# Optimization experiments

Measured on AMD Instinct MI355X. Metric: run time of the kernel, lower is better.

Reference implementation:

```python
import jax, jax.numpy as jnp
import numpy as np

ALPHA = 0.2
EMB_DIM = 128
IMG = 48


def setup_inputs() -> dict:
    key = jax.random.key(0)
    k1, k2, k3, k4 = jax.random.split(key, 4)
    B = 8192
    batch_anchor = jax.random.normal(k1, (B, 1, IMG, IMG), dtype=jnp.float32)
    batch_pos = jax.random.normal(k2, (B, 1, IMG, IMG), dtype=jnp.float32)
    batch_neg = jax.random.normal(k3, (B, 1, IMG, IMG), dtype=jnp.float32)
    W = jax.random.normal(k4, (IMG * IMG, EMB_DIM), dtype=jnp.float32) * (1.0 / np.sqrt(IMG * IMG))
    b = jnp.zeros((EMB_DIM,), dtype=jnp.float32)
    return {"batch_anchor": batch_anchor, "batch_pos": batch_pos, "batch_neg": batch_neg, "W": W, "b": b}


def _encode(x, W, b):
    # x: [B, 1, 48, 48] -> flatten -> linear -> [B, emb]
    B = x.shape[0]
    return x.reshape(B, -1) @ W + b


def reference(batch_anchor, batch_pos, batch_neg, W, b):
    emb_a = _encode(batch_anchor, W, b)
    emb_p = _encode(batch_pos, W, b)
    emb_n = _encode(batch_neg, W, b)
    d_ap = jnp.sum((emb_a - emb_p) ** 2, axis=-1)  # squared distance, [B]
    d_an = jnp.sum((emb_a - emb_n) ** 2, axis=-1)
    loss = jax.nn.relu(d_ap - d_an + ALPHA)
    return jnp.mean(loss)
```

## Files before the change

### kernel.cpp

```cpp
#include <hip/hip_runtime.h>


#define KDIM  2304
#define EMBD  128
#define BATCH 8192
#define NT    8
#define NW    8
#define CPW   9
#define ALPHA 0.2f

typedef __attribute__((ext_vector_type(8))) short short8;
typedef __attribute__((ext_vector_type(4))) float f32x4;
typedef __attribute__((ext_vector_type(4))) unsigned int u32x4;

#define AS1 __attribute__((address_space(1)))
#define AS3 __attribute__((address_space(3)))

__device__ __forceinline__ unsigned short f2bf(float f) {
    unsigned u = __builtin_bit_cast(unsigned, f);
    u += 0x7FFFu + ((u >> 16) & 1u);
    return (unsigned short)(u >> 16);
}

__global__ void pack_w_kernel(const float* __restrict__ W,
                              unsigned short* __restrict__ Wp) {
    int tid = blockIdx.x * blockDim.x + threadIdx.x;
    int n = tid & 127;
    int k = tid >> 7;
    int c = k >> 5;
    int q = (k >> 3) & 3;
    int j = k & 7;
    int t = n >> 4;
    int l = q * 16 + (n & 15);
    Wp[(size_t)(((c * 8 + t) * 64) + l) * 8 + j] = f2bf(W[tid]);
}

__device__ __forceinline__ unsigned cvtpk(float lo, float hi) {
    unsigned r;
    asm("v_cvt_pk_bf16_f32 %0, %1, %2" : "=v"(r) : "v"(lo), "v"(hi));
    return r;
}

__device__ __forceinline__ void gll16(const float* g, char* l) {
    __builtin_amdgcn_global_load_lds((AS1 void*)(void*)g, (AS3 void*)l, 16, 0, 0);
}

__device__ __forceinline__ void lds_read6(const char* p, f32x4& a0, f32x4& a1,
                                          f32x4& p0, f32x4& p1,
                                          f32x4& n0, f32x4& n1) {
    const AS3 char* lp = (const AS3 char*)p;
    asm volatile(
        "ds_read_b128 %0, %6 offset:0\n\t"
        "ds_read_b128 %1, %6 offset:1024\n\t"
        "ds_read_b128 %2, %6 offset:2048\n\t"
        "ds_read_b128 %3, %6 offset:3072\n\t"
        "ds_read_b128 %4, %6 offset:4096\n\t"
        "ds_read_b128 %5, %6 offset:5120\n\t"
        "s_waitcnt lgkmcnt(0)"
        : "=&v"(a0), "=&v"(a1), "=&v"(p0), "=&v"(p1), "=&v"(n0), "=&v"(n1)
        : "v"(lp)
        : "memory");
}

__global__ __launch_bounds__(512, 2) void triplet_kernel(
    const float* __restrict__ A, const float* __restrict__ P,
    const float* __restrict__ Ng, const unsigned short* __restrict__ Wp,
    float* __restrict__ out)
{
    __shared__ __align__(16) char smem[NW * 12288];

    const int lane = threadIdx.x & 63;
    const int wave = threadIdx.x >> 6;
    const int c0   = wave * CPW;

    const size_t goff = (size_t)(blockIdx.x * 16 + (lane & 15)) * KDIM
                      + (size_t)(lane >> 4) * 8 + (size_t)c0 * 32;
    const float* gA = A  + goff;
    const float* gP = P  + goff;
    const float* gN = Ng + goff;

    char* wb = smem + wave * 12288;

    const short8* wp = (const short8*)Wp + lane + (size_t)c0 * NT * 64;

    f32x4 aU[NT], aV[NT];
#pragma unroll
    for (int t = 0; t < NT; ++t) {
        aU[t] = (f32x4){0.f, 0.f, 0.f, 0.f};
        aV[t] = (f32x4){0.f, 0.f, 0.f, 0.f};
    }

#define STAGE(cc, bufoff)                                   \
    do {                                                    \
        const float* _a = gA + (cc) * 32;                   \
        const float* _p = gP + (cc) * 32;                   \
        const float* _n = gN + (cc) * 32;                   \
        char* _b = wb + (bufoff);                           \
        gll16(_a,     _b);                                  \
        gll16(_a + 4, _b + 1024);                           \
        gll16(_p,     _b + 2048);                           \
        gll16(_p + 4, _b + 3072);                           \
        gll16(_n,     _b + 4096);                           \
        gll16(_n + 4, _b + 5120);                           \
    } while (0)

    STAGE(0, 0);

    const char* rp0 = wb + lane * 16;
    const char* rp1 = wb + 6144 + lane * 16;

#pragma unroll
    for (int c = 0; c < CPW; ++c) {
        short8 wf[NT];
#pragma unroll
        for (int t = 0; t < NT; ++t) wf[t] = wp[c * 512 + t * 64];

        if (c + 1 < CPW) {
            STAGE(c + 1, ((c + 1) & 1) * 6144);
            asm volatile("s_waitcnt vmcnt(6)" ::: "memory");
        } else {
            asm volatile("s_waitcnt vmcnt(0)" ::: "memory");
        }

        f32x4 xa0, xa1, xp0, xp1, xn0, xn1;
        lds_read6((c & 1) ? rp1 : rp0, xa0, xa1, xp0, xp1, xn0, xn1);

        f32x4 ul = xa0 - xp0, uh = xa1 - xp1;
        f32x4 vl = xa0 - xn0, vh = xa1 - xn1;
        u32x4 uw, vw;
        uw[0] = cvtpk(ul[0], ul[1]); uw[1] = cvtpk(ul[2], ul[3]);
        uw[2] = cvtpk(uh[0], uh[1]); uw[3] = cvtpk(uh[2], uh[3]);
        vw[0] = cvtpk(vl[0], vl[1]); vw[1] = cvtpk(vl[2], vl[3]);
        vw[2] = cvtpk(vh[0], vh[1]); vw[3] = cvtpk(vh[2], vh[3]);
        short8 uf = __builtin_bit_cast(short8, uw);
        short8 vf = __builtin_bit_cast(short8, vw);

#pragma unroll
        for (int t = 0; t < NT; ++t) {
            aU[t] = __builtin_amdgcn_mfma_f32_16x16x32_bf16(uf, wf[t], aU[t], 0, 0, 0);
            aV[t] = __builtin_amdgcn_mfma_f32_16x16x32_bf16(vf, wf[t], aV[t], 0, 0, 0);
        }
    }

    __syncthreads();

    float (*lds)[2][NT][64][4] = (float(*)[2][NT][64][4])(void*)smem;

#define STORE_FRAGS(r)                                              \
    do {                                                            \
        _Pragma("unroll")                                           \
        for (int t = 0; t < NT; ++t) {                              \
            *(f32x4*)&lds[r][0][t][lane][0] = aU[t];                \
            *(f32x4*)&lds[r][1][t][lane][0] = aV[t];                \
        }                                                           \
    } while (0)
#define ADD_FRAGS(r)                                                \
    do {                                                            \
        _Pragma("unroll")                                           \
        for (int t = 0; t < NT; ++t) {                              \
            aU[t] += *(const f32x4*)&lds[r][0][t][lane][0];         \
            aV[t] += *(const f32x4*)&lds[r][1][t][lane][0];         \
        }                                                           \
    } while (0)

    if (wave >= 4) STORE_FRAGS(wave - 4);
    __syncthreads();
    if (wave < 4) ADD_FRAGS(wave);
    __syncthreads();
    if (wave == 2 || wave == 3) STORE_FRAGS(wave - 2);
    __syncthreads();
    if (wave < 2) ADD_FRAGS(wave);
    __syncthreads();
    if (wave == 1) STORE_FRAGS(0);
    __syncthreads();

    if (wave == 0) {
        ADD_FRAGS(0);
        float du[4] = {0.f, 0.f, 0.f, 0.f};
        float dv[4] = {0.f, 0.f, 0.f, 0.f};
#pragma unroll
        for (int t = 0; t < NT; ++t) {
#pragma unroll
            for (int r = 0; r < 4; ++r) {
                du[r] += aU[t][r] * aU[t][r];
                dv[r] += aV[t][r] * aV[t][r];
            }
        }
#pragma unroll
        for (int msk = 1; msk < 16; msk <<= 1) {
#pragma unroll
            for (int r = 0; r < 4; ++r) {
                du[r] += __shfl_xor(du[r], msk, 64);
                dv[r] += __shfl_xor(dv[r], msk, 64);
            }
        }
        float s = 0.f;
#pragma unroll
        for (int r = 0; r < 4; ++r) {
            float l = du[r] - dv[r] + ALPHA;
            s += l > 0.f ? l : 0.f;
        }
        s += __shfl_xor(s, 16, 64);
        s += __shfl_xor(s, 32, 64);
        if (lane == 0) atomicAdd(out, s * (1.0f / BATCH));
    }
}

extern "C" void kernel_launch(void* const* d_in, const int* in_sizes, int n_in,
                              void* d_out, int out_size, void* d_ws, size_t ws_size,
                              hipStream_t stream) {
    const float* A  = (const float*)d_in[0];
    const float* P  = (const float*)d_in[1];
    const float* Ng = (const float*)d_in[2];
    const float* W  = (const float*)d_in[3];
    unsigned short* Wp = (unsigned short*)d_ws;

    hipMemsetAsync(d_out, 0, sizeof(float), stream);

    pack_w_kernel<<<(KDIM * EMBD) / 256, 256, 0, stream>>>(W, Wp);
    triplet_kernel<<<BATCH / 16, 512, 0, stream>>>(A, P, Ng, Wp, (float*)d_out);
}
```

Measured before the change: 236.4 us.

## Process two row tiles per wave to reuse W fragments across rows

Each block now handles 32 batch rows with 4 waves instead of 16 rows with 8 waves, and each wave splits K into 18 chunks and computes two 16-row M-tiles. Every W fragment loaded from global memory is reused for two MFMA tiles, which halves W traffic per row, and the cross-wave LDS reduction loses one stage. In exchange the accumulator count doubles, so register pressure rises, launch bounds drop to one block per SM, and the grid shrinks to 256 blocks, which cuts occupancy and latency hiding for the streaming input loads.

New measurement: 234.5 us. About the same (-0.8%).

```diff
diff --git a/kernel.cpp b/kernel.cpp
--- a/kernel.cpp
+++ b/kernel.cpp
@@ -5,8 +5,9 @@
 #define EMBD  128
 #define BATCH 8192
 #define NT    8
-#define NW    8
-#define CPW   9
+#define NW    4
+#define MT    2
+#define CPW   18
 #define ALPHA 0.2f
 
 typedef __attribute__((ext_vector_type(8))) short short8;
@@ -62,52 +63,56 @@
         : "memory");
 }
 
-__global__ __launch_bounds__(512, 2) void triplet_kernel(
+__global__ __launch_bounds__(256, 1) void triplet_kernel(
     const float* __restrict__ A, const float* __restrict__ P,
     const float* __restrict__ Ng, const unsigned short* __restrict__ Wp,
     float* __restrict__ out)
 {
-    __shared__ __align__(16) char smem[NW * 12288];
+    __shared__ __align__(16) char smem[NW * 24576];
 
     const int lane = threadIdx.x & 63;
     const int wave = threadIdx.x >> 6;
     const int c0   = wave * CPW;
 
-    const size_t goff = (size_t)(blockIdx.x * 16 + (lane & 15)) * KDIM
-                      + (size_t)(lane >> 4) * 8 + (size_t)c0 * 32;
-    const float* gA = A  + goff;
-    const float* gP = P  + goff;
-    const float* gN = Ng + goff;
-
-    char* wb = smem + wave * 12288;
+    const size_t goff0 = (size_t)(blockIdx.x * 32 + (lane & 15)) * KDIM
+                       + (size_t)(lane >> 4) * 8 + (size_t)c0 * 32;
+    const size_t goff1 = goff0 + (size_t)16 * KDIM;
+    const float* gA0 = A  + goff0;  const float* gA1 = A  + goff1;
+    const float* gP0 = P  + goff0;  const float* gP1 = P  + goff1;
+    const float* gN0 = Ng + goff0;  const float* gN1 = Ng + goff1;
+
+    char* wb = smem + wave * 24576;
 
     const short8* wp = (const short8*)Wp + lane + (size_t)c0 * NT * 64;
 
-    f32x4 aU[NT], aV[NT];
-#pragma unroll
-    for (int t = 0; t < NT; ++t) {
-        aU[t] = (f32x4){0.f, 0.f, 0.f, 0.f};
-        aV[t] = (f32x4){0.f, 0.f, 0.f, 0.f};
-    }
+    f32x4 aU[MT][NT], aV[MT][NT];
+#pragma unroll
+    for (int mt = 0; mt < MT; ++mt)
+#pragma unroll
+        for (int t = 0; t < NT; ++t) {
+            aU[mt][t] = (f32x4){0.f, 0.f, 0.f, 0.f};
+            aV[mt][t] = (f32x4){0.f, 0.f, 0.f, 0.f};
+        }
 
 #define STAGE(cc, bufoff)                                   \
     do {                                                    \
-        const float* _a = gA + (cc) * 32;                   \
-        const float* _p = gP + (cc) * 32;                   \
-        const float* _n = gN + (cc) * 32;                   \
+        const int _o = (cc) * 32;                           \
         char* _b = wb + (bufoff);                           \
-        gll16(_a,     _b);                                  \
-        gll16(_a + 4, _b + 1024);                           \
-        gll16(_p,     _b + 2048);                           \
-        gll16(_p + 4, _b + 3072);                           \
-        gll16(_n,     _b + 4096);                           \
-        gll16(_n + 4, _b + 5120);                           \
+        gll16(gA0 + _o,     _b);                            \
+        gll16(gA0 + _o + 4, _b + 1024);                     \
+        gll16(gP0 + _o,     _b + 2048);                     \
+        gll16(gP0 + _o + 4, _b + 3072);                     \
+        gll16(gN0 + _o,     _b + 4096);                     \
+        gll16(gN0 + _o + 4, _b + 5120);                     \
+        gll16(gA1 + _o,     _b + 6144);                     \
+        gll16(gA1 + _o + 4, _b + 7168);                     \
+        gll16(gP1 + _o,     _b + 8192);                     \
+        gll16(gP1 + _o + 4, _b + 9216);                     \
+        gll16(gN1 + _o,     _b + 10240);                    \
+        gll16(gN1 + _o + 4, _b + 11264);                    \
     } while (0)
 
     STAGE(0, 0);
-
-    const char* rp0 = wb + lane * 16;
-    const char* rp1 = wb + 6144 + lane * 16;
 
 #pragma unroll
     for (int c = 0; c < CPW; ++c) {
@@ -116,58 +121,62 @@
         for (int t = 0; t < NT; ++t) wf[t] = wp[c * 512 + t * 64];
 
         if (c + 1 < CPW) {
-            STAGE(c + 1, ((c + 1) & 1) * 6144);
-            asm volatile("s_waitcnt vmcnt(6)" ::: "memory");
+            STAGE(c + 1, ((c + 1) & 1) * 12288);
+            asm volatile("s_waitcnt vmcnt(12)" ::: "memory");
         } else {
             asm volatile("s_waitcnt vmcnt(0)" ::: "memory");
         }
 
-        f32x4 xa0, xa1, xp0, xp1, xn0, xn1;
-        lds_read6((c & 1) ? rp1 : rp0, xa0, xa1, xp0, xp1, xn0, xn1);
-
-        f32x4 ul = xa0 - xp0, uh = xa1 - xp1;
-        f32x4 vl = xa0 - xn0, vh = xa1 - xn1;
-        u32x4 uw, vw;
-        uw[0] = cvtpk(ul[0], ul[1]); uw[1] = cvtpk(ul[2], ul[3]);
-        uw[2] = cvtpk(uh[0], uh[1]); uw[3] = cvtpk(uh[2], uh[3]);
-        vw[0] = cvtpk(vl[0], vl[1]); vw[1] = cvtpk(vl[2], vl[3]);
-        vw[2] = cvtpk(vh[0], vh[1]); vw[3] = cvtpk(vh[2], vh[3]);
-        short8 uf = __builtin_bit_cast(short8, uw);
-        short8 vf = __builtin_bit_cast(short8, vw);
-
-#pragma unroll
-        for (int t = 0; t < NT; ++t) {
-            aU[t] = __builtin_amdgcn_mfma_f32_16x16x32_bf16(uf, wf[t], aU[t], 0, 0, 0);
-            aV[t] = __builtin_amdgcn_mfma_f32_16x16x32_bf16(vf, wf[t], aV[t], 0, 0, 0);
+#pragma unroll
+        for (int mt = 0; mt < MT; ++mt) {
+            const char* rp = wb + (c & 1) * 12288 + mt * 6144 + lane * 16;
+            f32x4 xa0, xa1, xp0, xp1, xn0, xn1;
+            lds_read6(rp, xa0, xa1, xp0, xp1, xn0, xn1);
+
+            f32x4 ul = xa0 - xp0, uh = xa1 - xp1;
+            f32x4 vl = xa0 - xn0, vh = xa1 - xn1;
+            u32x4 uw, vw;
+            uw[0] = cvtpk(ul[0], ul[1]); uw[1] = cvtpk(ul[2], ul[3]);
+            uw[2] = cvtpk(uh[0], uh[1]); uw[3] = cvtpk(uh[2], uh[3]);
+            vw[0] = cvtpk(vl[0], vl[1]); vw[1] = cvtpk(vl[2], vl[3]);
+            vw[2] = cvtpk(vh[0], vh[1]); vw[3] = cvtpk(vh[2], vh[3]);
+            short8 uf = __builtin_bit_cast(short8, uw);
+            short8 vf = __builtin_bit_cast(short8, vw);
+
+#pragma unroll
+            for (int t = 0; t < NT; ++t) {
+                aU[mt][t] = __builtin_amdgcn_mfma_f32_16x16x32_bf16(uf, wf[t], aU[mt][t], 0, 0, 0);
+                aV[mt][t] = __builtin_amdgcn_mfma_f32_16x16x32_bf16(vf, wf[t], aV[mt][t], 0, 0, 0);
+            }
         }
     }
 
     __syncthreads();
 
-    float (*lds)[2][NT][64][4] = (float(*)[2][NT][64][4])(void*)smem;
+    float (*lds)[MT][2][NT][64][4] = (float(*)[MT][2][NT][64][4])(void*)smem;
 
 #define STORE_FRAGS(r)                                              \
     do {                                                            \
         _Pragma("unroll")                                           \
-        for (int t = 0; t < NT; ++t) {                              \
-            *(f32x4*)&lds[r][0][t][lane][0] = aU[t];                \
-            *(f32x4*)&lds[r][1][t][lane][0] = aV[t];                \
-        }                                                           \
+        for (int mt = 0; mt < MT; ++mt)                             \
+        { _Pragma("unroll")                                         \
+          for (int t = 0; t < NT; ++t) {                            \
+            *(f32x4*)&lds[r][mt][0][t][lane][0] = aU[mt][t];        \
+            *(f32x4*)&lds[r][mt][1][t][lane][0] = aV[mt][t];        \
+          } }                                                       \
     } while (0)
 #define ADD_FRAGS(r)                                                \
     do {                                                            \
         _Pragma("unroll")                                           \
-        for (int t = 0; t < NT; ++t) {                              \
-            aU[t] += *(const f32x4*)&lds[r][0][t][lane][0];         \
-            aV[t] += *(const f32x4*)&lds[r][1][t][lane][0];         \
-        }                                                           \
+        for (int mt = 0; mt < MT; ++mt)                             \
+        { _Pragma("unroll")                                         \
+          for (int t = 0; t < NT; ++t) {                            \
+            aU[mt][t] += *(const f32x4*)&lds[r][mt][0][t][lane][0]; \
+            aV[mt][t] += *(const f32x4*)&lds[r][mt][1][t][lane][0]; \
+          } }                                                       \
     } while (0)
 
-    if (wave >= 4) STORE_FRAGS(wave - 4);
-    __syncthreads();
-    if (wave < 4) ADD_FRAGS(wave);
-    __syncthreads();
-    if (wave == 2 || wave == 3) STORE_FRAGS(wave - 2);
+    if (wave >= 2) STORE_FRAGS(wave - 2);
     __syncthreads();
     if (wave < 2) ADD_FRAGS(wave);
     __syncthreads();
@@ -176,30 +185,37 @@
 
     if (wave == 0) {
         ADD_FRAGS(0);
-        float du[4] = {0.f, 0.f, 0.f, 0.f};
-        float dv[4] = {0.f, 0.f, 0.f, 0.f};
-#pragma unroll
-        for (int t = 0; t < NT; ++t) {
+        float du[MT][4], dv[MT][4];
+#pragma unroll
+        for (int mt = 0; mt < MT; ++mt)
+#pragma unroll
+            for (int r = 0; r < 4; ++r) { du[mt][r] = 0.f; dv[mt][r] = 0.f; }
+#pragma unroll
+        for (int mt = 0; mt < MT; ++mt)
+#pragma unroll
+            for (int t = 0; t < NT; ++t)
+#pragma unroll
+                for (int r = 0; r < 4; ++r) {
+                    du[mt][r] += aU[mt][t][r] * aU[mt][t][r];
+                    dv[mt][r] += aV[mt][t][r] * aV[mt][t][r];
+                }
+#pragma unroll
+        for (int msk = 1; msk < 16; msk <<= 1)
+#pragma unroll
+            for (int mt = 0; mt < MT; ++mt)
+#pragma unroll
+                for (int r = 0; r < 4; ++r) {
+                    du[mt][r] += __shfl_xor(du[mt][r], msk, 64);
+                    dv[mt][r] += __shfl_xor(dv[mt][r], msk, 64);
+                }
+        float s = 0.f;
+#pragma unroll
+        for (int mt = 0; mt < MT; ++mt)
 #pragma unroll
             for (int r = 0; r < 4; ++r) {
-                du[r] += aU[t][r] * aU[t][r];
-                dv[r] += aV[t][r] * aV[t][r];
+                float l = du[mt][r] - dv[mt][r] + ALPHA;
+                s += l > 0.f ? l : 0.f;
             }
-        }
-#pragma unroll
-        for (int msk = 1; msk < 16; msk <<= 1) {
-#pragma unroll
-            for (int r = 0; r < 4; ++r) {
-                du[r] += __shfl_xor(du[r], msk, 64);
-                dv[r] += __shfl_xor(dv[r], msk, 64);
-            }
-        }
-        float s = 0.f;
-#pragma unroll
-        for (int r = 0; r < 4; ++r) {
-            float l = du[r] - dv[r] + ALPHA;
-            s += l > 0.f ? l : 0.f;
-        }
         s += __shfl_xor(s, 16, 64);
         s += __shfl_xor(s, 32, 64);
         if (lane == 0) atomicAdd(out, s * (1.0f / BATCH));
@@ -218,5 +234,5 @@
     hipMemsetAsync(d_out, 0, sizeof(float), stream);
 
     pack_w_kernel<<<(KDIM * EMBD) / 256, 256, 0, stream>>>(W, Wp);
-    triplet_kernel<<<BATCH / 16, 512, 0, stream>>>(A, P, Ng, Wp, (float*)d_out);
-}
+    triplet_kernel<<<BATCH / 32, 256, 0, stream>>>(A, P, Ng, Wp, (float*)d_out);
+}
```

## Switch to 32x32x16 MFMA tiles with 32 rows per block and double-buffered W fragments

Applied to the files above, without the earlier changes.

Each block now handles 32 batch rows using 32x32x16 bf16 MFMAs over 4 output tiles, with 18 K-chunks per wave instead of 9. Each W fragment loaded from global memory is reused across twice as many rows, and the next chunk's W fragments are prefetched into a second register set alongside the LDS staging of the inputs. The cross-wave reduction is rewritten for the 16-element accumulators and runs separately for the U and V accumulators. The grid is halved, so there are fewer blocks and waves in flight to hide the latency of the memory-heavy input stream, and the accumulators use more registers.

Result: slower. 246.6 us (+4.3%).

```diff
diff --git a/kernel.cpp b/kernel.cpp
--- a/kernel.cpp
+++ b/kernel.cpp
@@ -4,13 +4,14 @@
 #define KDIM  2304
 #define EMBD  128
 #define BATCH 8192
-#define NT    8
+#define NT    4
 #define NW    8
-#define CPW   9
+#define CPW   18
 #define ALPHA 0.2f
 
 typedef __attribute__((ext_vector_type(8))) short short8;
 typedef __attribute__((ext_vector_type(4))) float f32x4;
+typedef __attribute__((ext_vector_type(16))) float f32x16;
 typedef __attribute__((ext_vector_type(4))) unsigned int u32x4;
 
 #define AS1 __attribute__((address_space(1)))
@@ -27,12 +28,12 @@
     int tid = blockIdx.x * blockDim.x + threadIdx.x;
     int n = tid & 127;
     int k = tid >> 7;
-    int c = k >> 5;
-    int q = (k >> 3) & 3;
+    int c = k >> 4;
+    int q = (k >> 3) & 1;
     int j = k & 7;
-    int t = n >> 4;
-    int l = q * 16 + (n & 15);
-    Wp[(size_t)(((c * 8 + t) * 64) + l) * 8 + j] = f2bf(W[tid]);
+    int t = n >> 5;
+    int l = q * 32 + (n & 31);
+    Wp[(size_t)(((c * 4 + t) * 64) + l) * 8 + j] = f2bf(W[tid]);
 }
 
 __device__ __forceinline__ unsigned cvtpk(float lo, float hi) {
@@ -73,134 +74,150 @@
     const int wave = threadIdx.x >> 6;
     const int c0   = wave * CPW;
 
-    const size_t goff = (size_t)(blockIdx.x * 16 + (lane & 15)) * KDIM
-                      + (size_t)(lane >> 4) * 8 + (size_t)c0 * 32;
+    const size_t goff = (size_t)(blockIdx.x * 32 + (lane & 31)) * KDIM
+                      + (size_t)((lane >> 5) * 8) + (size_t)c0 * 16;
     const float* gA = A  + goff;
     const float* gP = P  + goff;
     const float* gN = Ng + goff;
 
     char* wb = smem + wave * 12288;
 
-    const short8* wp = (const short8*)Wp + lane + (size_t)c0 * NT * 64;
-
-    f32x4 aU[NT], aV[NT];
+    const short8* wpw = (const short8*)Wp + lane + (size_t)c0 * 256;
+
+    f32x16 aU[NT], aV[NT];
 #pragma unroll
     for (int t = 0; t < NT; ++t) {
-        aU[t] = (f32x4){0.f, 0.f, 0.f, 0.f};
-        aV[t] = (f32x4){0.f, 0.f, 0.f, 0.f};
+#pragma unroll
+        for (int r = 0; r < 16; ++r) { aU[t][r] = 0.f; aV[t][r] = 0.f; }
     }
 
 #define STAGE(cc, bufoff)                                   \
     do {                                                    \
-        const float* _a = gA + (cc) * 32;                   \
-        const float* _p = gP + (cc) * 32;                   \
-        const float* _n = gN + (cc) * 32;                   \
+        const int _o = (cc) * 16;                           \
         char* _b = wb + (bufoff);                           \
-        gll16(_a,     _b);                                  \
-        gll16(_a + 4, _b + 1024);                           \
-        gll16(_p,     _b + 2048);                           \
-        gll16(_p + 4, _b + 3072);                           \
-        gll16(_n,     _b + 4096);                           \
-        gll16(_n + 4, _b + 5120);                           \
-    } while (0)
+        gll16(gA + _o,     _b);                             \
+        gll16(gA + _o + 4, _b + 1024);                      \
+        gll16(gP + _o,     _b + 2048);                      \
+        gll16(gP + _o + 4, _b + 3072);                      \
+        gll16(gN + _o,     _b + 4096);                      \
+        gll16(gN + _o + 4, _b + 5120);                      \
+    } while (0)
+
+#define LOADW(WF, cc)                                       \
+    do {                                                    \
+        _Pragma("unroll")                                   \
+        for (int t = 0; t < NT; ++t)                        \
+            WF[t] = wpw[(cc) * 256 + t * 64];               \
+    } while (0)
+
+#define COMPUTE(bufoff, WF)                                             \
+    do {                                                                \
+        f32x4 xa0, xa1, xp0, xp1, xn0, xn1;                             \
+        lds_read6(wb + (bufoff) + lane * 16, xa0, xa1, xp0, xp1, xn0, xn1); \
+        f32x4 ul = xa0 - xp0, uh = xa1 - xp1;                           \
+        f32x4 vl = xa0 - xn0, vh = xa1 - xn1;                           \
+        u32x4 uw, vw;                                                   \
+        uw[0] = cvtpk(ul[0], ul[1]); uw[1] = cvtpk(ul[2], ul[3]);       \
+        uw[2] = cvtpk(uh[0], uh[1]); uw[3] = cvtpk(uh[2], uh[3]);       \
+        vw[0] = cvtpk(vl[0], vl[1]); vw[1] = cvtpk(vl[2], vl[3]);       \
+        vw[2] = cvtpk(vh[0], vh[1]); vw[3] = cvtpk(vh[2], vh[3]);       \
+        short8 uf = __builtin_bit_cast(short8, uw);                     \
+        short8 vf = __builtin_bit_cast(short8, vw);                     \
+        _Pragma("unroll")                                               \
+        for (int t = 0; t < NT; ++t) {                                  \
+            aU[t] = __builtin_amdgcn_mfma_f32_32x32x16_bf16(uf, WF[t], aU[t], 0, 0, 0); \
+            aV[t] = __builtin_amdgcn_mfma_f32_32x32x16_bf16(vf, WF[t], aV[t], 0, 0, 0); \
+        }                                                               \
+    } while (0)
+
+    short8 wf0[NT], wf1[NT];
 
     STAGE(0, 0);
-
-    const char* rp0 = wb + lane * 16;
-    const char* rp1 = wb + 6144 + lane * 16;
+    LOADW(wf0, 0);
 
 #pragma unroll
     for (int c = 0; c < CPW; ++c) {
-        short8 wf[NT];
-#pragma unroll
-        for (int t = 0; t < NT; ++t) wf[t] = wp[c * 512 + t * 64];
-
+        short8* wfc = (c & 1) ? wf1 : wf0;
+        short8* wfn = (c & 1) ? wf0 : wf1;
         if (c + 1 < CPW) {
             STAGE(c + 1, ((c + 1) & 1) * 6144);
-            asm volatile("s_waitcnt vmcnt(6)" ::: "memory");
+            LOADW(wfn, c + 1);
+            asm volatile("s_waitcnt vmcnt(10)" ::: "memory");
         } else {
             asm volatile("s_waitcnt vmcnt(0)" ::: "memory");
         }
-
-        f32x4 xa0, xa1, xp0, xp1, xn0, xn1;
-        lds_read6((c & 1) ? rp1 : rp0, xa0, xa1, xp0, xp1, xn0, xn1);
-
-        f32x4 ul = xa0 - xp0, uh = xa1 - xp1;
-        f32x4 vl = xa0 - xn0, vh = xa1 - xn1;
-        u32x4 uw, vw;
-        uw[0] = cvtpk(ul[0], ul[1]); uw[1] = cvtpk(ul[2], ul[3]);
-        uw[2] = cvtpk(uh[0], uh[1]); uw[3] = cvtpk(uh[2], uh[3]);
-        vw[0] = cvtpk(vl[0], vl[1]); vw[1] = cvtpk(vl[2], vl[3]);
-        vw[2] = cvtpk(vh[0], vh[1]); vw[3] = cvtpk(vh[2], vh[3]);
-        short8 uf = __builtin_bit_cast(short8, uw);
-        short8 vf = __builtin_bit_cast(short8, vw);
-
-#pragma unroll
-        for (int t = 0; t < NT; ++t) {
-            aU[t] = __builtin_amdgcn_mfma_f32_16x16x32_bf16(uf, wf[t], aU[t], 0, 0, 0);
-            aV[t] = __builtin_amdgcn_mfma_f32_16x16x32_bf16(vf, wf[t], aV[t], 0, 0, 0);
-        }
+        COMPUTE((c & 1) * 6144, wfc);
     }
 
     __syncthreads();
 
-    float (*lds)[2][NT][64][4] = (float(*)[2][NT][64][4])(void*)smem;
-
-#define STORE_FRAGS(r)                                              \
-    do {                                                            \
-        _Pragma("unroll")                                           \
-        for (int t = 0; t < NT; ++t) {                              \
-            *(f32x4*)&lds[r][0][t][lane][0] = aU[t];                \
-            *(f32x4*)&lds[r][1][t][lane][0] = aV[t];                \
-        }                                                           \
-    } while (0)
-#define ADD_FRAGS(r)                                                \
-    do {                                                            \
-        _Pragma("unroll")                                           \
-        for (int t = 0; t < NT; ++t) {                              \
-            aU[t] += *(const f32x4*)&lds[r][0][t][lane][0];         \
-            aV[t] += *(const f32x4*)&lds[r][1][t][lane][0];         \
-        }                                                           \
-    } while (0)
-
-    if (wave >= 4) STORE_FRAGS(wave - 4);
-    __syncthreads();
-    if (wave < 4) ADD_FRAGS(wave);
-    __syncthreads();
-    if (wave == 2 || wave == 3) STORE_FRAGS(wave - 2);
-    __syncthreads();
-    if (wave < 2) ADD_FRAGS(wave);
-    __syncthreads();
-    if (wave == 1) STORE_FRAGS(0);
-    __syncthreads();
+#define STOREX(ACC, r)                                                  \
+    do {                                                                \
+        _Pragma("unroll")                                               \
+        for (int t = 0; t < NT; ++t) {                                  \
+            _Pragma("unroll")                                           \
+            for (int q = 0; q < 4; ++q) {                               \
+                f32x4 piece = {ACC[t][q*4+0], ACC[t][q*4+1],            \
+                               ACC[t][q*4+2], ACC[t][q*4+3]};           \
+                *(f32x4*)(smem + (r)*16384 + t*4096 + lane*64 + q*16) = piece; \
+            }                                                           \
+        }                                                               \
+    } while (0)
+#define ADDX(ACC, r)                                                    \
+    do {                                                                \
+        _Pragma("unroll")                                               \
+        for (int t = 0; t < NT; ++t) {                                  \
+            _Pragma("unroll")                                           \
+            for (int q = 0; q < 4; ++q) {                               \
+                f32x4 piece = *(const f32x4*)(smem + (r)*16384 + t*4096 + lane*64 + q*16); \
+                ACC[t][q*4+0] += piece[0]; ACC[t][q*4+1] += piece[1];   \
+                ACC[t][q*4+2] += piece[2]; ACC[t][q*4+3] += piece[3];   \
+            }                                                           \
+        }                                                               \
+    } while (0)
+#define TREE(ACC)                                                       \
+    do {                                                                \
+        if (wave >= 4) STOREX(ACC, wave - 4);                           \
+        __syncthreads();                                                \
+        if (wave < 4) ADDX(ACC, wave);                                  \
+        __syncthreads();                                                \
+        if (wave == 2 || wave == 3) STOREX(ACC, wave - 2);              \
+        __syncthreads();                                                \
+        if (wave < 2) ADDX(ACC, wave);                                  \
+        __syncthreads();                                                \
+        if (wave == 1) STOREX(ACC, 0);                                  \
+        __syncthreads();                                                \
+        if (wave == 0) ADDX(ACC, 0);                                    \
+        __syncthreads();                                                \
+    } while (0)
+
+    TREE(aU);
+    TREE(aV);
 
     if (wave == 0) {
-        ADD_FRAGS(0);
-        float du[4] = {0.f, 0.f, 0.f, 0.f};
-        float dv[4] = {0.f, 0.f, 0.f, 0.f};
-#pragma unroll
-        for (int t = 0; t < NT; ++t) {
-#pragma unroll
-            for (int r = 0; r < 4; ++r) {
+        float du[16], dv[16];
+#pragma unroll
+        for (int r = 0; r < 16; ++r) { du[r] = 0.f; dv[r] = 0.f; }
+#pragma unroll
+        for (int t = 0; t < NT; ++t)
+#pragma unroll
+            for (int r = 0; r < 16; ++r) {
                 du[r] += aU[t][r] * aU[t][r];
                 dv[r] += aV[t][r] * aV[t][r];
             }
-        }
-#pragma unroll
-        for (int msk = 1; msk < 16; msk <<= 1) {
-#pragma unroll
-            for (int r = 0; r < 4; ++r) {
+#pragma unroll
+        for (int msk = 1; msk < 32; msk <<= 1)
+#pragma unroll
+            for (int r = 0; r < 16; ++r) {
                 du[r] += __shfl_xor(du[r], msk, 64);
                 dv[r] += __shfl_xor(dv[r], msk, 64);
             }
-        }
         float s = 0.f;
 #pragma unroll
-        for (int r = 0; r < 4; ++r) {
+        for (int r = 0; r < 16; ++r) {
             float l = du[r] - dv[r] + ALPHA;
             s += l > 0.f ? l : 0.f;
         }
-        s += __shfl_xor(s, 16, 64);
         s += __shfl_xor(s, 32, 64);
         if (lane == 0) atomicAdd(out, s * (1.0f / BATCH));
     }
@@ -218,5 +235,5 @@
     hipMemsetAsync(d_out, 0, sizeof(float), stream);
 
     pack_w_kernel<<<(KDIM * EMBD) / 256, 256, 0, stream>>>(W, Wp);
-    triplet_kernel<<<BATCH / 16, 512, 0, stream>>>(A, P, Ng, Wp, (float*)d_out);
-}
+    triplet_kernel<<<BATCH / 32, 512, 0, stream>>>(A, P, Ng, Wp, (float*)d_out);
+}
```
